# Kernel optimization log

Measured on AMD Instinct MI355X. Metric: run time of the kernel, lower is better.

Reference implementation:

```python
import jax, jax.numpy as jnp
import numpy as np

B, S, E, H = 2, 2048, 2048, 32
D = E // H
SCALE = D ** -0.5
LN_EPS = 1e-5
NEG = -1e9  # finite large-negative for masked logits (avoids NaN grads)


def setup_inputs() -> dict:
    key = jax.random.key(0)
    ks = jax.random.split(key, 12)
    hidden_states = jax.random.normal(ks[0], (B, S, E), dtype=jnp.float32)
    # additive causal mask, shape (B, 1, S, S) as the module requires
    causal = jnp.where(jnp.tril(jnp.ones((S, S), dtype=bool)), 0.0, NEG).astype(jnp.float32)
    attention_mask = jnp.broadcast_to(causal[None, None], (B, 1, S, S))
    p = lambda k: jax.random.normal(k, (E, E), dtype=jnp.float32) * 0.02
    Wq, Wk, Wv, Wo = p(ks[1]), p(ks[2]), p(ks[3]), p(ks[4])
    bq = jax.random.normal(ks[5], (E,), dtype=jnp.float32) * 0.02
    bk = jax.random.normal(ks[6], (E,), dtype=jnp.float32) * 0.02
    bv = jax.random.normal(ks[7], (E,), dtype=jnp.float32) * 0.02
    bo = jax.random.normal(ks[8], (E,), dtype=jnp.float32) * 0.02
    ln_gamma = jnp.ones((E,), dtype=jnp.float32)
    ln_beta = jnp.zeros((E,), dtype=jnp.float32)
    return {"hidden_states": hidden_states, "attention_mask": attention_mask,
            "Wq": Wq, "bq": bq, "Wk": Wk, "bk": bk, "Wv": Wv, "bv": bv,
            "Wo": Wo, "bo": bo, "ln_gamma": ln_gamma, "ln_beta": ln_beta}


def _shape(x):  # [B,S,E] -> [B,H,S,D]
    return x.reshape(B, S, H, D).transpose(0, 2, 1, 3)


def reference(hidden_states, attention_mask, Wq, bq, Wk, bk, Wv, bv, Wo, bo, ln_gamma, ln_beta):
    q = _shape((hidden_states @ Wq.T + bq) * SCALE)   # [B,H,S,D]
    k = _shape(hidden_states @ Wk.T + bk)
    v = _shape(hidden_states @ Wv.T + bv)
    attn_weights = jnp.einsum('bhsd,bhtd->bhst', q, k) + attention_mask
    attn_weights = jax.nn.softmax(attn_weights, axis=-1)
    ctx = jnp.einsum('bhst,bhtd->bhsd', attn_weights, v)  # [B,H,S,D]
    ctx = ctx.transpose(0, 2, 1, 3).reshape(B, S, E)
    # inner attention LayerNorm
    mu = jnp.mean(ctx, axis=-1, keepdims=True)
    var = jnp.var(ctx, axis=-1, keepdims=True)
    ctx = (ctx - mu) * jax.lax.rsqrt(var + LN_EPS) * ln_gamma + ln_beta
    return ctx @ Wo.T + bo
```

## Files before the change

### kernel.cpp

```cpp
#include <hip/hip_runtime.h>
#include <hip/hip_bf16.h>
#include <cstdint>
#include <cstddef>

#define BB 2
#define SEQ 2048
#define EMB 2048
#define NH 32
#define HD 64
#define QSCALE2 0.18033688011112042f

#if __has_builtin(__builtin_amdgcn_exp2f)
#define EXP2(x) __builtin_amdgcn_exp2f(x)
#else
#define EXP2(x) exp2f(x)
#endif

typedef __hip_bfloat16 bf16;
typedef __attribute__((ext_vector_type(8))) short short8;
typedef __attribute__((ext_vector_type(4))) float floatx4;

__device__ __forceinline__ floatx4 mfma16(short8 a, short8 b, floatx4 c) {
    return __builtin_amdgcn_mfma_f32_16x16x32_bf16(a, b, c, 0, 0, 0);
}

__device__ __forceinline__ void gl_lds16(const void* g, void* s) {
    __builtin_amdgcn_global_load_lds((const __attribute__((address_space(1))) void*)g,
                                     (__attribute__((address_space(3))) void*)s,
                                     16, 0, 0);
}

__global__ __launch_bounds__(256) void f2b(const float4* __restrict__ x,
                                           uint2* __restrict__ y, int n4) {
    int i = blockIdx.x * 256 + threadIdx.x;
    if (i >= n4) return;
    float4 v = x[i];
    union { bf16 h[4]; uint2 u; } p;
    p.h[0] = __float2bfloat16(v.x);
    p.h[1] = __float2bfloat16(v.y);
    p.h[2] = __float2bfloat16(v.z);
    p.h[3] = __float2bfloat16(v.w);
    y[i] = p.u;
}

__global__ __launch_bounds__(256) void f2b4(const float4* __restrict__ w0,
                                            const float4* __restrict__ w1,
                                            const float4* __restrict__ w2,
                                            const float4* __restrict__ w3,
                                            uint2* __restrict__ y, int n4) {
    int i = blockIdx.x * 256 + threadIdx.x;
    if (i >= n4) return;
    const float4* src = (blockIdx.y == 0) ? w0 : (blockIdx.y == 1) ? w1
                      : (blockIdx.y == 2) ? w2 : w3;
    float4 v = src[i];
    union { bf16 h[4]; uint2 u; } p;
    p.h[0] = __float2bfloat16(v.x);
    p.h[1] = __float2bfloat16(v.y);
    p.h[2] = __float2bfloat16(v.z);
    p.h[3] = __float2bfloat16(v.w);
    y[(size_t)blockIdx.y * n4 + i] = p.u;
}

__device__ __forceinline__ void store_out(bf16* p, float v)  { *p = __float2bfloat16(v); }
__device__ __forceinline__ void store_out(float* p, float v) { *p = v; }

template <typename OutT, bool BROW>
__global__ __launch_bounds__(256, 2) void gemm_bt(
    const bf16* __restrict__ A, const bf16* __restrict__ W,
    const float* __restrict__ bias, OutT* __restrict__ C,
    int M, int N, int K, float scale)
{
    __shared__ bf16 As[128 * 32];
    __shared__ bf16 Bs[128 * 32];

    const int tid  = threadIdx.x;
    const int wid  = tid >> 6;
    const int lane = tid & 63;
    const int quad = lane >> 4;
    const int l16  = lane & 15;
    const int wr   = wid >> 1;
    const int wc   = wid & 1;
    const int row0 = blockIdx.y * 128;
    const int col0 = blockIdx.x * 128;

    floatx4 acc[4][4] = {};

    for (int kb = 0; kb < K; kb += 32) {
#pragma unroll
        for (int i = 0; i < 2; ++i) {
            int l = tid + i * 256;
            int r = l >> 2;
            int kp = (l & 3) << 3;
            gl_lds16(A + (size_t)(row0 + r) * K + kb + kp, &As[l * 8]);
        }
#pragma unroll
        for (int i = 0; i < 2; ++i) {
            int l = tid + i * 256;
            int r = l >> 2;
            int kp = (l & 3) << 3;
            gl_lds16(W + (size_t)(col0 + r) * K + kb + kp, &Bs[l * 8]);
        }
        __syncthreads();

        short8 af[4], bfm[4];
#pragma unroll
        for (int i = 0; i < 4; ++i)
            af[i] = *(const short8*)&As[(wr * 64 + i * 16 + l16) * 32 + quad * 8];
#pragma unroll
        for (int j = 0; j < 4; ++j)
            bfm[j] = *(const short8*)&Bs[(wc * 64 + j * 16 + l16) * 32 + quad * 8];
#pragma unroll
        for (int i = 0; i < 4; ++i)
#pragma unroll
            for (int j = 0; j < 4; ++j)
                acc[i][j] = mfma16(af[i], bfm[j], acc[i][j]);
        __syncthreads();
    }

#pragma unroll
    for (int i = 0; i < 4; ++i) {
        int row = row0 + wr * 64 + i * 16 + quad * 4;
#pragma unroll
        for (int j = 0; j < 4; ++j) {
            int col = col0 + wc * 64 + j * 16 + l16;
            float bc = BROW ? 0.f : bias[col];
#pragma unroll
            for (int r = 0; r < 4; ++r) {
                float bb = BROW ? bias[row + r] : bc;
                float v = (acc[i][j][r] + bb) * scale;
                store_out(&C[(size_t)(row + r) * N + col], v);
            }
        }
    }
}

__global__ __launch_bounds__(256, 2) void gemm_qk(
    const bf16* __restrict__ A, const bf16* __restrict__ W,
    const float* __restrict__ bq, const float* __restrict__ bk,
    bf16* __restrict__ Qo, bf16* __restrict__ Ko, int K)
{
    __shared__ bf16 As[128 * 32];
    __shared__ bf16 Bs[128 * 32];

    const int tid  = threadIdx.x;
    const int wid  = tid >> 6;
    const int lane = tid & 63;
    const int quad = lane >> 4;
    const int l16  = lane & 15;
    const int wr   = wid >> 1;
    const int wc   = wid & 1;
    const int row0 = blockIdx.y * 128;
    const int col0 = blockIdx.x * 128;

    floatx4 acc[4][4] = {};

    for (int kb = 0; kb < K; kb += 32) {
#pragma unroll
        for (int i = 0; i < 2; ++i) {
            int l = tid + i * 256;
            int r = l >> 2;
            int kp = (l & 3) << 3;
            gl_lds16(A + (size_t)(row0 + r) * K + kb + kp, &As[l * 8]);
        }
#pragma unroll
        for (int i = 0; i < 2; ++i) {
            int l = tid + i * 256;
            int r = l >> 2;
            int kp = (l & 3) << 3;
            gl_lds16(W + (size_t)(col0 + r) * K + kb + kp, &Bs[l * 8]);
        }
        __syncthreads();

        short8 af[4], bfm[4];
#pragma unroll
        for (int i = 0; i < 4; ++i)
            af[i] = *(const short8*)&As[(wr * 64 + i * 16 + l16) * 32 + quad * 8];
#pragma unroll
        for (int j = 0; j < 4; ++j)
            bfm[j] = *(const short8*)&Bs[(wc * 64 + j * 16 + l16) * 32 + quad * 8];
#pragma unroll
        for (int i = 0; i < 4; ++i)
#pragma unroll
            for (int j = 0; j < 4; ++j)
                acc[i][j] = mfma16(af[i], bfm[j], acc[i][j]);
        __syncthreads();
    }

    const bool isQ = (col0 < EMB);
    bf16* base = isQ ? Qo : Ko;
    const float* bias = isQ ? bq : bk;
    const float sc = isQ ? QSCALE2 : 1.f;
    const int cb = isQ ? col0 : col0 - EMB;

#pragma unroll
    for (int i = 0; i < 4; ++i) {
        int row = row0 + wr * 64 + i * 16 + quad * 4;
#pragma unroll
        for (int j = 0; j < 4; ++j) {
            int col = cb + wc * 64 + j * 16 + l16;
            float b = bias[col];
#pragma unroll
            for (int r = 0; r < 4; ++r) {
                float v = (acc[i][j][r] + b) * sc;
                base[(size_t)(row + r) * EMB + col] = __float2bfloat16(v);
            }
        }
    }
}

__global__ __launch_bounds__(256, 3) void attn(
    const bf16* __restrict__ Q, const bf16* __restrict__ K,
    const bf16* __restrict__ Vt, bf16* __restrict__ ctx)
{
    const int bh   = blockIdx.x;
    const int pair = blockIdx.y;
    const int b    = bh >> 5;
    const int h    = bh & 31;
    const int tid  = threadIdx.x;
    const int wid  = tid >> 6;
    const int lane = tid & 63;
    const int quad = lane >> 4;
    const int l16  = lane & 15;
    const int NT   = SEQ / 128;

    __shared__ bf16 Ks[2][64 * 64];
    __shared__ bf16 Vts[2][64 * 64];
    __shared__ bf16 Ps[4][32 * 72];

    const size_t bhoff = (size_t)b * SEQ * EMB + (size_t)h * HD;
    const size_t vtoff = (size_t)(h * HD) * (BB * SEQ) + (size_t)b * SEQ;

    short8 ones;
#pragma unroll
    for (int i = 0; i < 8; ++i) ones[i] = (short)0x3F80;

#define STAGE(kc, bufi)                                                         \
    {                                                                           \
        _Pragma("unroll")                                                       \
        for (int i = 0; i < 2; ++i) {                                           \
            int l = tid + i * 256;                                              \
            int r8 = l >> 3;                                                    \
            int g = (((l & 7) ^ (r8 & 7)) << 3);                                \
            gl_lds16(K + bhoff + (size_t)((kc) * 64 + r8) * EMB + g,            \
                     &Ks[bufi][l * 8]);                                         \
        }                                                                       \
        _Pragma("unroll")                                                       \
        for (int i = 0; i < 2; ++i) {                                           \
            int l = tid + i * 256;                                              \
            int r8 = l >> 3;                                                    \
            int g = (((l & 7) ^ (r8 & 7)) << 3);                                \
            gl_lds16(Vt + vtoff + (size_t)r8 * (BB * SEQ) + (kc) * 64 + g,      \
                     &Vts[bufi][l * 8]);                                        \
        }                                                                       \
    }

    for (int t = 0; t < 2; ++t) {
        const int qt = t ? pair : (NT - 1 - pair);
        const int qbase = qt * 128;

        short8 qf[2][2];
#pragma unroll
        for (int mi = 0; mi < 2; ++mi) {
            int qrow = qbase + wid * 32 + mi * 16 + l16;
            const bf16* qp = Q + bhoff + (size_t)qrow * EMB + quad * 8;
            qf[mi][0] = *(const short8*)qp;
            qf[mi][1] = *(const short8*)(qp + 32);
        }

        floatx4 o[2][4] = {};
        floatx4 ol[2] = {};
        int tb[2];
        tb[0] = (qbase + wid * 32) >> 6;
        tb[1] = (qbase + wid * 32 + 16) >> 6;
        const int nchunks = 2 * qt + 2;

        __syncthreads();
        STAGE(0, 0);

        for (int kc = 0; kc < nchunks; ++kc) {
            const int buf = kc & 1;
            __syncthreads();
            if (kc + 1 < nchunks) STAGE(kc + 1, buf ^ 1);

            floatx4 s[2][4];
#pragma unroll
            for (int n = 0; n < 4; ++n) {
                int row = n * 16 + l16;
                int sw = l16 & 7;
                short8 kf0 = *(const short8*)&Ks[buf][row * 64 + ((quad ^ sw) << 3)];
                short8 kf1 = *(const short8*)&Ks[buf][row * 64 + (((quad + 4) ^ sw) << 3)];
#pragma unroll
                for (int mi = 0; mi < 2; ++mi) {
                    floatx4 z = {};
                    s[mi][n] = mfma16(qf[mi][1], kf1, mfma16(qf[mi][0], kf0, z));
                }
            }

#pragma unroll
            for (int mi = 0; mi < 2; ++mi) {
                if (kc >= tb[mi]) {
                    int rbase = qbase + wid * 32 + mi * 16 + quad * 4;
#pragma unroll
                    for (int n = 0; n < 4; ++n) {
                        int key = kc * 64 + n * 16 + l16;
#pragma unroll
                        for (int r = 0; r < 4; ++r)
                            if (key > rbase + r) s[mi][n][r] = -1e9f;
                    }
                }
#pragma unroll
                for (int n = 0; n < 4; ++n)
#pragma unroll
                    for (int r = 0; r < 4; ++r)
                        Ps[wid][(mi * 16 + quad * 4 + r) * 72 + n * 16 + l16] =
                            __float2bfloat16(EXP2(s[mi][n][r]));
            }

            short8 pf[2][2];
#pragma unroll
            for (int mi = 0; mi < 2; ++mi) {
                pf[mi][0] = *(const short8*)&Ps[wid][(mi * 16 + l16) * 72 + quad * 8];
                pf[mi][1] = *(const short8*)&Ps[wid][(mi * 16 + l16) * 72 + 32 + quad * 8];
            }
#pragma unroll
            for (int n = 0; n < 4; ++n) {
                int row = n * 16 + l16;
                int sw = l16 & 7;
                short8 vf0 = *(const short8*)&Vts[buf][row * 64 + ((quad ^ sw) << 3)];
                short8 vf1 = *(const short8*)&Vts[buf][row * 64 + (((quad + 4) ^ sw) << 3)];
#pragma unroll
                for (int mi = 0; mi < 2; ++mi)
                    o[mi][n] = mfma16(pf[mi][1], vf1, mfma16(pf[mi][0], vf0, o[mi][n]));
            }
#pragma unroll
            for (int mi = 0; mi < 2; ++mi)
                ol[mi] = mfma16(pf[mi][1], ones, mfma16(pf[mi][0], ones, ol[mi]));
        }

#pragma unroll
        for (int mi = 0; mi < 2; ++mi)
#pragma unroll
            for (int r = 0; r < 4; ++r) {
                int grow = qbase + wid * 32 + mi * 16 + quad * 4 + r;
                float inv = 1.f / ol[mi][r];
#pragma unroll
                for (int n = 0; n < 4; ++n)
                    ctx[bhoff + (size_t)grow * EMB + n * 16 + l16] =
                        __float2bfloat16(o[mi][n][r] * inv);
            }
    }
#undef STAGE
}

__global__ __launch_bounds__(256) void lnorm(
    const bf16* __restrict__ ctx, const float* __restrict__ gamma,
    const float* __restrict__ beta, bf16* __restrict__ out)
{
    const int row = blockIdx.x;
    const bf16* x = ctx + (size_t)row * EMB;
    float v[8];
    float s = 0.f, ss = 0.f;
#pragma unroll
    for (int i = 0; i < 8; ++i) {
        v[i] = __bfloat162float(x[threadIdx.x + i * 256]);
        s += v[i];
        ss += v[i] * v[i];
    }
#pragma unroll
    for (int off = 1; off < 64; off <<= 1) {
        s  += __shfl_xor(s, off);
        ss += __shfl_xor(ss, off);
    }
    __shared__ float red[2][4];
    int wid = threadIdx.x >> 6, lane = threadIdx.x & 63;
    if (lane == 0) { red[0][wid] = s; red[1][wid] = ss; }
    __syncthreads();
    s  = red[0][0] + red[0][1] + red[0][2] + red[0][3];
    ss = red[1][0] + red[1][1] + red[1][2] + red[1][3];
    float mu  = s * (1.f / EMB);
    float var = ss * (1.f / EMB) - mu * mu;
    float rs  = rsqrtf(var + 1e-5f);
    bf16* y = out + (size_t)row * EMB;
#pragma unroll
    for (int i = 0; i < 8; ++i) {
        int c = threadIdx.x + i * 256;
        y[c] = __float2bfloat16((v[i] - mu) * rs * gamma[c] + beta[c]);
    }
}

extern "C" void kernel_launch(void* const* d_in, const int* in_sizes, int n_in,
                              void* d_out, int out_size, void* d_ws, size_t ws_size,
                              hipStream_t stream) {
    const float* X     = (const float*)d_in[0];
    const float* Wq    = (const float*)d_in[2];
    const float* bq    = (const float*)d_in[3];
    const float* Wk    = (const float*)d_in[4];
    const float* bk    = (const float*)d_in[5];
    const float* Wv    = (const float*)d_in[6];
    const float* bv    = (const float*)d_in[7];
    const float* Wo    = (const float*)d_in[8];
    const float* bo    = (const float*)d_in[9];
    const float* gamma = (const float*)d_in[10];
    const float* beta  = (const float*)d_in[11];
    float* out = (float*)d_out;

    const size_t M  = (size_t)BB * SEQ;
    const size_t ME = M * EMB;
    const size_t EE = (size_t)EMB * EMB;

    const size_t need = (ME + 4 * EE + ME + ME) * sizeof(bf16);
    if (ws_size < need) return;

    bf16* Xb   = (bf16*)d_ws;
    bf16* Wqb  = Xb  + ME;
    bf16* Wkb  = Wqb + EE;
    bf16* Wvb  = Wkb + EE;
    bf16* Wob  = Wvb + EE;
    bf16* Vt   = Wob + EE;
    bf16* ctxn = Vt  + ME;
    bf16* Qb   = (bf16*)d_out;
    bf16* Kb   = Qb + ME;
    bf16* ctx  = Qb;

    dim3 blk(256);
    f2b<<<dim3((unsigned)(ME / 4 / 256)), blk, 0, stream>>>((const float4*)X, (uint2*)Xb, ME / 4);
    f2b4<<<dim3((unsigned)(EE / 4 / 256), 4), blk, 0, stream>>>(
        (const float4*)Wq, (const float4*)Wk, (const float4*)Wv, (const float4*)Wo,
        (uint2*)Wqb, EE / 4);

    dim3 gqk(2 * EMB / 128, M / 128);
    dim3 gg(EMB / 128, M / 128);
    dim3 gg2(M / 128, EMB / 128);
    gemm_qk<<<gqk, blk, 0, stream>>>(Xb, Wqb, bq, bk, Qb, Kb, EMB);
    gemm_bt<bf16, true ><<<gg2, blk, 0, stream>>>(Wvb, Xb, bv, Vt, EMB, M, EMB, 1.f);
    attn<<<dim3(BB * NH, SEQ / 256), blk, 0, stream>>>(Qb, Kb, Vt, ctx);
    lnorm<<<dim3((unsigned)M), blk, 0, stream>>>(ctx, gamma, beta, ctxn);
    gemm_bt<float, false><<<gg, blk, 0, stream>>>(ctxn, Wob, bo, out, M, EMB, EMB, 1.f);
}
```

Before: 401.7 us.

## Fuse conversions and QKV GEMMs, widen K-tile to 64 with swizzled LDS

Merges the two fp32-to-bf16 conversion kernels into one launch and folds the Q/K and transposed-V projections into a single GEMM grid of 48x32 blocks. The GEMM kernels now stage a 64-wide K slice per iteration instead of 32, which halves the number of barrier pairs, and they use an XOR swizzle on the LDS layout to cut bank conflicts on fragment reads. This removes launch overhead and the tail effect between the QK and V launches. The cost is twice the LDS per block, which may limit occupancy, and hardcoded size constants that only fit this problem shape.

New measurement: 375.7 us. -6.5%, faster.

```diff
diff --git a/kernel.cpp b/kernel.cpp
--- a/kernel.cpp
+++ b/kernel.cpp
@@ -30,123 +30,147 @@
                                      16, 0, 0);
 }
 
-__global__ __launch_bounds__(256) void f2b(const float4* __restrict__ x,
-                                           uint2* __restrict__ y, int n4) {
+#define NX4 2097152
+#define NW4 1048576
+__global__ __launch_bounds__(256) void f2ball(
+    const float4* __restrict__ X,  const float4* __restrict__ Wq,
+    const float4* __restrict__ Wk, const float4* __restrict__ Wv,
+    const float4* __restrict__ Wo, uint2* __restrict__ dst) {
     int i = blockIdx.x * 256 + threadIdx.x;
-    if (i >= n4) return;
-    float4 v = x[i];
+    const float4* src;
+    int si;
+    if (i < NX4) { src = X; si = i; }
+    else {
+        int j = i - NX4;
+        int w = j >> 20;
+        si = j & (NW4 - 1);
+        src = (w == 0) ? Wq : (w == 1) ? Wk : (w == 2) ? Wv : Wo;
+    }
+    float4 v = src[si];
     union { bf16 h[4]; uint2 u; } p;
     p.h[0] = __float2bfloat16(v.x);
     p.h[1] = __float2bfloat16(v.y);
     p.h[2] = __float2bfloat16(v.z);
     p.h[3] = __float2bfloat16(v.w);
-    y[i] = p.u;
-}
-
-__global__ __launch_bounds__(256) void f2b4(const float4* __restrict__ w0,
-                                            const float4* __restrict__ w1,
-                                            const float4* __restrict__ w2,
-                                            const float4* __restrict__ w3,
-                                            uint2* __restrict__ y, int n4) {
-    int i = blockIdx.x * 256 + threadIdx.x;
-    if (i >= n4) return;
-    const float4* src = (blockIdx.y == 0) ? w0 : (blockIdx.y == 1) ? w1
-                      : (blockIdx.y == 2) ? w2 : w3;
-    float4 v = src[i];
-    union { bf16 h[4]; uint2 u; } p;
-    p.h[0] = __float2bfloat16(v.x);
-    p.h[1] = __float2bfloat16(v.y);
-    p.h[2] = __float2bfloat16(v.z);
-    p.h[3] = __float2bfloat16(v.w);
-    y[(size_t)blockIdx.y * n4 + i] = p.u;
-}
-
-__device__ __forceinline__ void store_out(bf16* p, float v)  { *p = __float2bfloat16(v); }
-__device__ __forceinline__ void store_out(float* p, float v) { *p = v; }
-
-template <typename OutT, bool BROW>
-__global__ __launch_bounds__(256, 2) void gemm_bt(
-    const bf16* __restrict__ A, const bf16* __restrict__ W,
-    const float* __restrict__ bias, OutT* __restrict__ C,
-    int M, int N, int K, float scale)
+    dst[i] = p.u;
+}
+
+#define GSTAGE(SRC, R0, KSTR, DST)                                        \
+    _Pragma("unroll")                                                     \
+    for (int i_ = 0; i_ < 4; ++i_) {                                      \
+        int l_ = tid + i_ * 256;                                          \
+        int r_ = l_ >> 3;                                                 \
+        int g_ = ((l_ & 7) ^ (r_ & 7)) << 3;                              \
+        gl_lds16(SRC + (size_t)((R0) + r_) * (KSTR) + kb + g_, &DST[l_ * 8]); \
+    }
+
+__device__ __forceinline__ short8 frag64(const bf16* S, int row, int grp, int sw) {
+    return *(const short8*)&S[row * 64 + ((grp ^ sw) << 3)];
+}
+
+__global__ __launch_bounds__(256, 2) void gemm_qkv(
+    const bf16* __restrict__ Xb, const bf16* __restrict__ Wqk,
+    const bf16* __restrict__ Wv,
+    const float* __restrict__ bq, const float* __restrict__ bk,
+    const float* __restrict__ bv,
+    bf16* __restrict__ Qo, bf16* __restrict__ Ko, bf16* __restrict__ Vt)
 {
-    __shared__ bf16 As[128 * 32];
-    __shared__ bf16 Bs[128 * 32];
+    __shared__ bf16 As[128 * 64];
+    __shared__ bf16 Bs[128 * 64];
+
+    const int bx = blockIdx.x, by = blockIdx.y;
+    const bool isV = (bx >= 32);
+    const bf16* Ap; const bf16* Wp; int row0, col0;
+    if (!isV) { Ap = Xb; row0 = by * 128;        Wp = Wqk; col0 = bx * 128; }
+    else      { Ap = Wv; row0 = (bx - 32) * 128; Wp = Xb;  col0 = by * 128; }
 
     const int tid  = threadIdx.x;
     const int wid  = tid >> 6;
     const int lane = tid & 63;
     const int quad = lane >> 4;
     const int l16  = lane & 15;
+    const int sw   = l16 & 7;
     const int wr   = wid >> 1;
     const int wc   = wid & 1;
-    const int row0 = blockIdx.y * 128;
-    const int col0 = blockIdx.x * 128;
 
     floatx4 acc[4][4] = {};
 
-    for (int kb = 0; kb < K; kb += 32) {
-#pragma unroll
-        for (int i = 0; i < 2; ++i) {
-            int l = tid + i * 256;
-            int r = l >> 2;
-            int kp = (l & 3) << 3;
-            gl_lds16(A + (size_t)(row0 + r) * K + kb + kp, &As[l * 8]);
-        }
-#pragma unroll
-        for (int i = 0; i < 2; ++i) {
-            int l = tid + i * 256;
-            int r = l >> 2;
-            int kp = (l & 3) << 3;
-            gl_lds16(W + (size_t)(col0 + r) * K + kb + kp, &Bs[l * 8]);
-        }
+    for (int kb = 0; kb < EMB; kb += 64) {
+        GSTAGE(Ap, row0, EMB, As);
+        GSTAGE(Wp, col0, EMB, Bs);
         __syncthreads();
 
-        short8 af[4], bfm[4];
-#pragma unroll
-        for (int i = 0; i < 4; ++i)
-            af[i] = *(const short8*)&As[(wr * 64 + i * 16 + l16) * 32 + quad * 8];
-#pragma unroll
-        for (int j = 0; j < 4; ++j)
-            bfm[j] = *(const short8*)&Bs[(wc * 64 + j * 16 + l16) * 32 + quad * 8];
-#pragma unroll
-        for (int i = 0; i < 4; ++i)
-#pragma unroll
-            for (int j = 0; j < 4; ++j)
-                acc[i][j] = mfma16(af[i], bfm[j], acc[i][j]);
+        short8 af[4][2], bfm[4][2];
+#pragma unroll
+        for (int i = 0; i < 4; ++i) {
+            int row = wr * 64 + i * 16 + l16;
+            af[i][0] = frag64(As, row, quad, sw);
+            af[i][1] = frag64(As, row, quad + 4, sw);
+        }
+#pragma unroll
+        for (int j = 0; j < 4; ++j) {
+            int row = wc * 64 + j * 16 + l16;
+            bfm[j][0] = frag64(Bs, row, quad, sw);
+            bfm[j][1] = frag64(Bs, row, quad + 4, sw);
+        }
+#pragma unroll
+        for (int kh = 0; kh < 2; ++kh)
+#pragma unroll
+            for (int i = 0; i < 4; ++i)
+#pragma unroll
+                for (int j = 0; j < 4; ++j)
+                    acc[i][j] = mfma16(af[i][kh], bfm[j][kh], acc[i][j]);
         __syncthreads();
     }
 
-#pragma unroll
-    for (int i = 0; i < 4; ++i) {
-        int row = row0 + wr * 64 + i * 16 + quad * 4;
-#pragma unroll
-        for (int j = 0; j < 4; ++j) {
-            int col = col0 + wc * 64 + j * 16 + l16;
-            float bc = BROW ? 0.f : bias[col];
-#pragma unroll
-            for (int r = 0; r < 4; ++r) {
-                float bb = BROW ? bias[row + r] : bc;
-                float v = (acc[i][j][r] + bb) * scale;
-                store_out(&C[(size_t)(row + r) * N + col], v);
-            }
-        }
-    }
-}
-
-__global__ __launch_bounds__(256, 2) void gemm_qk(
+    if (!isV) {
+        const bool isQ = (bx < 16);
+        bf16* base = isQ ? Qo : Ko;
+        const float* bias = isQ ? bq : bk;
+        const float sc = isQ ? QSCALE2 : 1.f;
+        const int cb = isQ ? col0 : col0 - EMB;
+#pragma unroll
+        for (int i = 0; i < 4; ++i) {
+            int row = row0 + wr * 64 + i * 16 + quad * 4;
+#pragma unroll
+            for (int j = 0; j < 4; ++j) {
+                int col = cb + wc * 64 + j * 16 + l16;
+                float b = bias[col];
+#pragma unroll
+                for (int r = 0; r < 4; ++r)
+                    base[(size_t)(row + r) * EMB + col] =
+                        __float2bfloat16((acc[i][j][r] + b) * sc);
+            }
+        }
+    } else {
+#pragma unroll
+        for (int i = 0; i < 4; ++i) {
+            int frow = row0 + wr * 64 + i * 16 + quad * 4;
+#pragma unroll
+            for (int j = 0; j < 4; ++j) {
+                int tok = col0 + wc * 64 + j * 16 + l16;
+#pragma unroll
+                for (int r = 0; r < 4; ++r)
+                    Vt[(size_t)(frow + r) * (BB * SEQ) + tok] =
+                        __float2bfloat16(acc[i][j][r] + bv[frow + r]);
+            }
+        }
+    }
+}
+
+__global__ __launch_bounds__(256, 2) void gemm_out(
     const bf16* __restrict__ A, const bf16* __restrict__ W,
-    const float* __restrict__ bq, const float* __restrict__ bk,
-    bf16* __restrict__ Qo, bf16* __restrict__ Ko, int K)
+    const float* __restrict__ bias, float* __restrict__ C)
 {
-    __shared__ bf16 As[128 * 32];
-    __shared__ bf16 Bs[128 * 32];
+    __shared__ bf16 As[128 * 64];
+    __shared__ bf16 Bs[128 * 64];
 
     const int tid  = threadIdx.x;
     const int wid  = tid >> 6;
     const int lane = tid & 63;
     const int quad = lane >> 4;
     const int l16  = lane & 15;
+    const int sw   = l16 & 7;
     const int wr   = wid >> 1;
     const int wc   = wid & 1;
     const int row0 = blockIdx.y * 128;
@@ -154,56 +178,44 @@
 
     floatx4 acc[4][4] = {};
 
-    for (int kb = 0; kb < K; kb += 32) {
-#pragma unroll
-        for (int i = 0; i < 2; ++i) {
-            int l = tid + i * 256;
-            int r = l >> 2;
-            int kp = (l & 3) << 3;
-            gl_lds16(A + (size_t)(row0 + r) * K + kb + kp, &As[l * 8]);
-        }
-#pragma unroll
-        for (int i = 0; i < 2; ++i) {
-            int l = tid + i * 256;
-            int r = l >> 2;
-            int kp = (l & 3) << 3;
-            gl_lds16(W + (size_t)(col0 + r) * K + kb + kp, &Bs[l * 8]);
-        }
+    for (int kb = 0; kb < EMB; kb += 64) {
+        GSTAGE(A, row0, EMB, As);
+        GSTAGE(W, col0, EMB, Bs);
         __syncthreads();
 
-        short8 af[4], bfm[4];
-#pragma unroll
-        for (int i = 0; i < 4; ++i)
-            af[i] = *(const short8*)&As[(wr * 64 + i * 16 + l16) * 32 + quad * 8];
-#pragma unroll
-        for (int j = 0; j < 4; ++j)
-            bfm[j] = *(const short8*)&Bs[(wc * 64 + j * 16 + l16) * 32 + quad * 8];
-#pragma unroll
-        for (int i = 0; i < 4; ++i)
-#pragma unroll
-            for (int j = 0; j < 4; ++j)
-                acc[i][j] = mfma16(af[i], bfm[j], acc[i][j]);
+        short8 af[4][2], bfm[4][2];
+#pragma unroll
+        for (int i = 0; i < 4; ++i) {
+            int row = wr * 64 + i * 16 + l16;
+            af[i][0] = frag64(As, row, quad, sw);
+            af[i][1] = frag64(As, row, quad + 4, sw);
+        }
+#pragma unroll
+        for (int j = 0; j < 4; ++j) {
+            int row = wc * 64 + j * 16 + l16;
+            bfm[j][0] = frag64(Bs, row, quad, sw);
+            bfm[j][1] = frag64(Bs, row, quad + 4, sw);
+        }
+#pragma unroll
+        for (int kh = 0; kh < 2; ++kh)
+#pragma unroll
+            for (int i = 0; i < 4; ++i)
+#pragma unroll
+                for (int j = 0; j < 4; ++j)
+                    acc[i][j] = mfma16(af[i][kh], bfm[j][kh], acc[i][j]);
         __syncthreads();
     }
-
-    const bool isQ = (col0 < EMB);
-    bf16* base = isQ ? Qo : Ko;
-    const float* bias = isQ ? bq : bk;
-    const float sc = isQ ? QSCALE2 : 1.f;
-    const int cb = isQ ? col0 : col0 - EMB;
 
 #pragma unroll
     for (int i = 0; i < 4; ++i) {
         int row = row0 + wr * 64 + i * 16 + quad * 4;
 #pragma unroll
         for (int j = 0; j < 4; ++j) {
-            int col = cb + wc * 64 + j * 16 + l16;
+            int col = col0 + wc * 64 + j * 16 + l16;
             float b = bias[col];
 #pragma unroll
-            for (int r = 0; r < 4; ++r) {
-                float v = (acc[i][j][r] + b) * sc;
-                base[(size_t)(row + r) * EMB + col] = __float2bfloat16(v);
-            }
+            for (int r = 0; r < 4; ++r)
+                C[(size_t)(row + r) * EMB + col] = acc[i][j][r] + b;
         }
     }
 }
@@ -418,22 +430,18 @@
     bf16* Wob  = Wvb + EE;
     bf16* Vt   = Wob + EE;
     bf16* ctxn = Vt  + ME;
+    (void)Wkb;
     bf16* Qb   = (bf16*)d_out;
     bf16* Kb   = Qb + ME;
     bf16* ctx  = Qb;
 
     dim3 blk(256);
-    f2b<<<dim3((unsigned)(ME / 4 / 256)), blk, 0, stream>>>((const float4*)X, (uint2*)Xb, ME / 4);
-    f2b4<<<dim3((unsigned)(EE / 4 / 256), 4), blk, 0, stream>>>(
-        (const float4*)Wq, (const float4*)Wk, (const float4*)Wv, (const float4*)Wo,
-        (uint2*)Wqb, EE / 4);
-
-    dim3 gqk(2 * EMB / 128, M / 128);
-    dim3 gg(EMB / 128, M / 128);
-    dim3 gg2(M / 128, EMB / 128);
-    gemm_qk<<<gqk, blk, 0, stream>>>(Xb, Wqb, bq, bk, Qb, Kb, EMB);
-    gemm_bt<bf16, true ><<<gg2, blk, 0, stream>>>(Wvb, Xb, bv, Vt, EMB, M, EMB, 1.f);
+    f2ball<<<dim3((NX4 + 4 * NW4) / 256), blk, 0, stream>>>(
+        (const float4*)X, (const float4*)Wq, (const float4*)Wk,
+        (const float4*)Wv, (const float4*)Wo, (uint2*)d_ws);
+
+    gemm_qkv<<<dim3(48, 32), blk, 0, stream>>>(Xb, Wqb, Wvb, bq, bk, bv, Qb, Kb, Vt);
     attn<<<dim3(BB * NH, SEQ / 256), blk, 0, stream>>>(Qb, Kb, Vt, ctx);
     lnorm<<<dim3((unsigned)M), blk, 0, stream>>>(ctx, gamma, beta, ctxn);
-    gemm_bt<float, false><<<gg, blk, 0, stream>>>(ctxn, Wob, bo, out, M, EMB, EMB, 1.f);
-}
+    gemm_out<<<dim3(EMB / 128, M / 128), blk, 0, stream>>>(ctxn, Wob, bo, out);
+}
```
